# Optimization experiments

Measured on AMD Instinct MI355X. Metric: run time of the kernel, lower is better.

## Reference

```python
import jax, jax.numpy as jnp
import numpy as np

H = 512          # size_half
K = 16           # n_segments
B = 8192         # batch
WIDTH = 1.0 / K  # spline bin width


def setup_inputs() -> dict:
    key = jax.random.key(0)
    ks = jax.random.split(key, 4)
    v_in = jax.random.uniform(ks[0], (B, 2 * H), dtype=jnp.float32)  # config in [0,1]
    log_density = jax.random.normal(ks[1], (B, 1), dtype=jnp.float32)
    W1 = jax.random.normal(ks[2], (H, H), dtype=jnp.float32) * (1.0 / np.sqrt(H))
    b1 = jnp.zeros((H,), dtype=jnp.float32)
    W2 = jax.random.normal(ks[3], (H, H * K), dtype=jnp.float32) * (1.0 / np.sqrt(H))
    b2 = jnp.zeros((H * K,), dtype=jnp.float32)
    return {"v_in": v_in, "log_density": log_density, "W1": W1, "b1": b1, "W2": W2, "b2": b2}


def reference(v_in, log_density, W1, b1, W2, b2):
    # even_sites=True: passive = first half, active = second half
    v_passive = v_in[:, :H]           # [B, H]
    v_active = v_in[:, H:]            # [B, H]

    # FullyConnectedNeuralNetwork: hidden layer + final layer, tanh activation on both
    h = jnp.tanh((v_passive - 0.5) @ W1 + b1)          # [B, H]
    net = jnp.tanh(h @ W2 + b2).reshape(-1, H, K)      # [B, H, K]
    p = jax.nn.softmax(net, axis=2)                    # bin probability masses P_k

    # y-coordinates of knots: CDF of the bin masses, with leading zero
    knots_y = jnp.concatenate(
        [jnp.zeros((p.shape[0], H, 1), p.dtype), jnp.cumsum(p, axis=2)], axis=2
    )                                                  # [B, H, K+1]

    # searchsorted on uniform knots linspace(0,1,K+1), then -1, clamped
    knots_x = jnp.linspace(0.0, 1.0, K + 1, dtype=v_in.dtype)
    k = jnp.clip(jnp.searchsorted(knots_x, v_active, side="left") - 1, 0, K - 1)  # [B, H]

    p_k = jnp.take_along_axis(p, k[..., None], axis=2)[..., 0]        # [B, H]
    y_lo = jnp.take_along_axis(knots_y, k[..., None], axis=2)[..., 0]  # [B, H]

    alpha = (v_active - k.astype(v_in.dtype) * WIDTH) / WIDTH          # [B, H]
    v_out_active = y_lo + alpha * p_k

    v_out = jnp.concatenate([v_passive, v_out_active], axis=1)         # [B, 2H]
    log_density_out = log_density - jnp.sum(jnp.log(p_k), axis=1, keepdims=True)  # [B, 1]
    return v_out, log_density_out
```

## Files before the change

### kernel.cpp

```cpp
#include <hip/hip_runtime.h>
#include <hip/hip_bf16.h>

#define HH   512
#define BB   8192
#define WIDTH (1.0f/16.0f)

typedef __attribute__((ext_vector_type(8))) short  short8;
typedef __attribute__((ext_vector_type(4))) float  floatx4;

typedef const __attribute__((address_space(1))) void* gptr_t;
typedef __attribute__((address_space(3))) void*       lptr_t;

__device__ __forceinline__ void gload_lds16(const void* g, void* l) {
    __builtin_amdgcn_global_load_lds((gptr_t)g, (lptr_t)l, 16, 0, 0);
}

__device__ __forceinline__ float tanh_fast(float x) {
    float e = __expf(2.0f * x);
    return 1.0f - 2.0f * __builtin_amdgcn_rcpf(e + 1.0f);
}

__global__ void prep_all(const float* __restrict__ vin, const float* __restrict__ W1,
                         const float* __restrict__ W2, const float* __restrict__ ld,
                         float* __restrict__ vout, float* __restrict__ ldout,
                         __hip_bfloat16* __restrict__ Abf,
                         __hip_bfloat16* __restrict__ W1T,
                         __hip_bfloat16* __restrict__ W2T) {
    __shared__ float tile[32][33];
    int bid = blockIdx.x, tid = threadIdx.x;
    if (bid < 4352) {
        const float* src;  __hip_bfloat16* dst;  int cols, c0, r0;
        if (bid < 4096) { src = W2; dst = W2T; cols = 8192; c0 = (bid & 255) * 32; r0 = (bid >> 8) * 32; }
        else            { int b = bid - 4096; src = W1; dst = W1T; cols = 512; c0 = (b & 15) * 32; r0 = (b >> 4) * 32; }
        int x = tid & 31, y = tid >> 5;
        #pragma unroll
        for (int i = 0; i < 32; i += 8)
            tile[y + i][x] = src[(size_t)(r0 + y + i) * cols + c0 + x];
        __syncthreads();
        #pragma unroll
        for (int i = 0; i < 32; i += 8)
            dst[(size_t)(c0 + y + i) * 512 + r0 + x] = __float2bfloat16(tile[x][y + i]);
    } else {
        int b = bid - 4352;
        int i = b * 256 + tid;
        int r = i >> 6, c = i & 63;
        const float4* src = (const float4*)(vin + (size_t)r * 1024 + c * 8);
        float4 f0 = src[0], f1 = src[1];
        float4* dst = (float4*)(vout + (size_t)r * 1024 + c * 8);
        dst[0] = f0; dst[1] = f1;
        union { __hip_bfloat16 h[8]; uint4 v; } u;
        u.h[0] = __float2bfloat16(f0.x - 0.5f); u.h[1] = __float2bfloat16(f0.y - 0.5f);
        u.h[2] = __float2bfloat16(f0.z - 0.5f); u.h[3] = __float2bfloat16(f0.w - 0.5f);
        u.h[4] = __float2bfloat16(f1.x - 0.5f); u.h[5] = __float2bfloat16(f1.y - 0.5f);
        u.h[6] = __float2bfloat16(f1.z - 0.5f); u.h[7] = __float2bfloat16(f1.w - 0.5f);
        *(uint4*)(Abf + (size_t)r * 512 + c * 8) = u.v;
        if (tid < 4) { int row = b * 4 + tid; ldout[row] = ld[row]; }
    }
}

__global__ __launch_bounds__(256, 4) void gemm1_kernel(
        const __hip_bfloat16* __restrict__ Abf,
        const __hip_bfloat16* __restrict__ W1T,
        const float* __restrict__ b1,
        __hip_bfloat16* __restrict__ hM) {
    __shared__ short ldsA[64 * 32];
    __shared__ short ldsB[128 * 32];
    int tid = threadIdx.x;
    int lane = tid & 63;
    int wv = tid >> 6, wr = wv >> 1, wc = wv & 1;
    int q = lane >> 4, cx = lane & 15;
    int rowBase = blockIdx.y * 64;
    int colBase = blockIdx.x * 128;
    floatx4 acc[2][4] = {};

    for (int k0 = 0; k0 < HH; k0 += 32) {
        {
            int row = tid >> 2, kc = tid & 3;
            unsigned loff = __builtin_amdgcn_readfirstlane((unsigned)((tid & 192) * 16));
            gload_lds16(Abf + (size_t)(rowBase + row) * HH + k0 + kc * 8, (char*)ldsA + loff);
        }
        #pragma unroll
        for (int j = 0; j < 2; ++j) {
            int i = j * 256 + tid;
            int row = i >> 2, kc = i & 3;
            unsigned loff = __builtin_amdgcn_readfirstlane((unsigned)((j * 256 + (tid & 192)) * 16));
            gload_lds16(W1T + (size_t)(colBase + row) * HH + k0 + kc * 8, (char*)ldsB + loff);
        }
        __syncthreads();
        short8 a[2], b[4];
        #pragma unroll
        for (int mt = 0; mt < 2; ++mt)
            a[mt] = *(const short8*)(ldsA + (wr * 32 + mt * 16 + cx) * 32 + q * 8);
        #pragma unroll
        for (int nt = 0; nt < 4; ++nt)
            b[nt] = *(const short8*)(ldsB + (wc * 64 + nt * 16 + cx) * 32 + q * 8);
        #pragma unroll
        for (int mt = 0; mt < 2; ++mt)
            #pragma unroll
            for (int nt = 0; nt < 4; ++nt)
                acc[mt][nt] = __builtin_amdgcn_mfma_f32_16x16x32_bf16(a[mt], b[nt], acc[mt][nt], 0, 0, 0);
        __syncthreads();
    }

    float b1v[4];
    #pragma unroll
    for (int nt = 0; nt < 4; ++nt) b1v[nt] = b1[colBase + wc * 64 + nt * 16 + cx];
    #pragma unroll
    for (int mt = 0; mt < 2; ++mt)
        #pragma unroll
        for (int nt = 0; nt < 4; ++nt) {
            int col = colBase + wc * 64 + nt * 16 + cx;
            #pragma unroll
            for (int r = 0; r < 4; ++r) {
                int row = rowBase + wr * 32 + mt * 16 + q * 4 + r;
                hM[(size_t)row * HH + col] = __float2bfloat16(tanh_fast(acc[mt][nt][r] + b1v[nt]));
            }
        }
}

__global__ __launch_bounds__(256, 4) void gemm2_kernel(
        const __hip_bfloat16* __restrict__ hM,
        const __hip_bfloat16* __restrict__ W2T,
        const float* __restrict__ b2,
        const float* __restrict__ vin,
        float* __restrict__ vout,
        float* __restrict__ ldout) {
    __shared__ __align__(16) char smem[32768];
    short* ldsA = (short*)smem;
    short* ldsB = (short*)(smem + 16384);
    float* ldsE = (float*)smem;
    int tid = threadIdx.x;
    int lane = tid & 63;
    int wv = tid >> 6, wr = wv >> 1, wc = wv & 1;
    int q = lane >> 4, cx = lane & 15;
    int rowBase = blockIdx.y * 128;
    int colBase = blockIdx.x * 128;
    floatx4 acc[4][4] = {};

    int aoff = (q ^ (cx & 3)) * 8;

    for (int k0 = 0; k0 < HH; k0 += 64) {
        #pragma unroll
        for (int j = 0; j < 4; ++j) {
            int chunk = j * 256 + tid;
            int half  = j >> 1;
            int c2    = chunk & 511;
            int row = c2 >> 2, kc = c2 & 3;
            int kcs = kc ^ (row & 3);
            unsigned loff = __builtin_amdgcn_readfirstlane((unsigned)((j * 256 + (tid & 192)) * 16));
            gload_lds16(hM  + (size_t)(rowBase + row) * HH + k0 + half * 32 + kcs * 8, (char*)ldsA + loff);
            gload_lds16(W2T + (size_t)(colBase + row) * HH + k0 + half * 32 + kcs * 8, (char*)ldsB + loff);
        }
        __syncthreads();
        #pragma unroll
        for (int s = 0; s < 2; ++s) {
            const short* pA = ldsA + s * 4096;
            const short* pB = ldsB + s * 4096;
            short8 a[4], b[4];
            #pragma unroll
            for (int mt = 0; mt < 4; ++mt)
                a[mt] = *(const short8*)(pA + (wr * 64 + mt * 16 + cx) * 32 + aoff);
            #pragma unroll
            for (int nt = 0; nt < 4; ++nt)
                b[nt] = *(const short8*)(pB + (wc * 64 + nt * 16 + cx) * 32 + aoff);
            #pragma unroll
            for (int mt = 0; mt < 4; ++mt)
                #pragma unroll
                for (int nt = 0; nt < 4; ++nt)
                    acc[mt][nt] = __builtin_amdgcn_mfma_f32_16x16x32_bf16(a[mt], b[nt], acc[mt][nt], 0, 0, 0);
        }
        __syncthreads();
    }

    float b2v[4];
    #pragma unroll
    for (int nt = 0; nt < 4; ++nt) b2v[nt] = b2[colBase + wc * 64 + nt * 16 + cx];

    float* myTile = ldsE + wv * (16 * 68);
    int rowL  = lane & 15;
    int gL    = lane >> 4;
    int gAbs  = blockIdx.x * 8 + wc * 4 + gL;

    #pragma unroll
    for (int mt = 0; mt < 4; ++mt) {
        #pragma unroll
        for (int nt = 0; nt < 4; ++nt)
            #pragma unroll
            for (int r = 0; r < 4; ++r)
                myTile[(q * 4 + r) * 68 + nt * 16 + cx] = acc[mt][nt][r] + b2v[nt];

        floatx4 x0 = *(const floatx4*)(myTile + rowL * 68 + gL * 16);
        floatx4 x1 = *(const floatx4*)(myTile + rowL * 68 + gL * 16 + 4);
        floatx4 x2 = *(const floatx4*)(myTile + rowL * 68 + gL * 16 + 8);
        floatx4 x3 = *(const floatx4*)(myTile + rowL * 68 + gL * 16 + 12);
        float xs[16] = { x0[0],x0[1],x0[2],x0[3], x1[0],x1[1],x1[2],x1[3],
                         x2[0],x2[1],x2[2],x2[3], x3[0],x3[1],x3[2],x3[3] };

        int row = rowBase + wr * 64 + mt * 16 + rowL;
        float v = vin[(size_t)row * 1024 + 512 + gAbs];
        int k = (int)ceilf(v * 16.0f) - 1;
        k = min(15, max(0, k));

        float s = 0.0f, csum = 0.0f, ek = 0.0f;
        #pragma unroll
        for (int j = 0; j < 16; ++j) {
            float e2 = __expf(2.0f * xs[j]);
            float t  = 1.0f - 2.0f * __builtin_amdgcn_rcpf(e2 + 1.0f);
            float e  = __expf(t);
            csum += (j < k)  ? e : 0.0f;
            ek    = (j == k) ? e : ek;
            s += e;
        }
        float rs = __builtin_amdgcn_rcpf(s);
        float pk  = ek * rs;
        float ylo = csum * rs;
        float alpha = (v - (float)k * WIDTH) * 16.0f;
        vout[(size_t)row * 1024 + 512 + gAbs] = ylo + alpha * pk;

        float logp = __logf(pk);
        logp += __shfl_xor(logp, 16, 64);
        logp += __shfl_xor(logp, 32, 64);
        if (lane < 16) atomicAdd(ldout + row, -logp);
    }
}

extern "C" void kernel_launch(void* const* d_in, const int* in_sizes, int n_in,
                              void* d_out, int out_size, void* d_ws, size_t ws_size,
                              hipStream_t stream) {
    const float* vin = (const float*)d_in[0];
    const float* ld  = (const float*)d_in[1];
    const float* W1  = (const float*)d_in[2];
    const float* b1  = (const float*)d_in[3];
    const float* W2  = (const float*)d_in[4];
    const float* b2  = (const float*)d_in[5];
    float* vout  = (float*)d_out;
    float* ldout = vout + (size_t)BB * 1024;

    char* ws = (char*)d_ws;
    __hip_bfloat16* Abf = (__hip_bfloat16*)(ws);
    __hip_bfloat16* W1T = (__hip_bfloat16*)(ws + 8388608);
    __hip_bfloat16* W2T = (__hip_bfloat16*)(ws + 8912896);
    __hip_bfloat16* hM  = (__hip_bfloat16*)(ws + 17301504);

    prep_all<<<6400, 256, 0, stream>>>(vin, W1, W2, ld, vout, ldout, Abf, W1T, W2T);
    gemm1_kernel<<<dim3(4, 128), 256, 0, stream>>>(Abf, W1T, b1, hM);
    gemm2_kernel<<<dim3(64, 64), 256, 0, stream>>>(hM, W2T, b2, vin, vout, ldout);
}
```

Before: 207.4 us.

## Use 32x32 MFMA in gemm2 and replace log-density atomics with partial-sum reduction

```diff
diff --git a/kernel.cpp b/kernel.cpp
--- a/kernel.cpp
+++ b/kernel.cpp
@@ -5,8 +5,9 @@
 #define BB   8192
 #define WIDTH (1.0f/16.0f)
 
-typedef __attribute__((ext_vector_type(8))) short  short8;
-typedef __attribute__((ext_vector_type(4))) float  floatx4;
+typedef __attribute__((ext_vector_type(8)))  short short8;
+typedef __attribute__((ext_vector_type(4)))  float floatx4;
+typedef __attribute__((ext_vector_type(16))) float floatx16;
 
 typedef const __attribute__((address_space(1))) void* gptr_t;
 typedef __attribute__((address_space(3))) void*       lptr_t;
@@ -21,8 +22,8 @@
 }
 
 __global__ void prep_all(const float* __restrict__ vin, const float* __restrict__ W1,
-                         const float* __restrict__ W2, const float* __restrict__ ld,
-                         float* __restrict__ vout, float* __restrict__ ldout,
+                         const float* __restrict__ W2,
+                         float* __restrict__ vout,
                          __hip_bfloat16* __restrict__ Abf,
                          __hip_bfloat16* __restrict__ W1T,
                          __hip_bfloat16* __restrict__ W2T) {
@@ -54,7 +55,6 @@
         u.h[4] = __float2bfloat16(f1.x - 0.5f); u.h[5] = __float2bfloat16(f1.y - 0.5f);
         u.h[6] = __float2bfloat16(f1.z - 0.5f); u.h[7] = __float2bfloat16(f1.w - 0.5f);
         *(uint4*)(Abf + (size_t)r * 512 + c * 8) = u.v;
-        if (tid < 4) { int row = b * 4 + tid; ldout[row] = ld[row]; }
     }
 }
 
@@ -124,20 +124,20 @@
         const float* __restrict__ b2,
         const float* __restrict__ vin,
         float* __restrict__ vout,
-        float* __restrict__ ldout) {
-    __shared__ __align__(16) char smem[32768];
+        float* __restrict__ partial) {
+    __shared__ __align__(16) char smem[34816];
     short* ldsA = (short*)smem;
     short* ldsB = (short*)(smem + 16384);
     float* ldsE = (float*)smem;
     int tid = threadIdx.x;
     int lane = tid & 63;
     int wv = tid >> 6, wr = wv >> 1, wc = wv & 1;
-    int q = lane >> 4, cx = lane & 15;
+    int m31 = lane & 31, q2 = lane >> 5;
     int rowBase = blockIdx.y * 128;
     int colBase = blockIdx.x * 128;
-    floatx4 acc[4][4] = {};
-
-    int aoff = (q ^ (cx & 3)) * 8;
+    floatx16 acc[2][2] = {};
+
+    int key = (lane & 3);
 
     for (int k0 = 0; k0 < HH; k0 += 64) {
         #pragma unroll
@@ -145,83 +145,102 @@
             int chunk = j * 256 + tid;
             int half  = j >> 1;
             int c2    = chunk & 511;
-            int row = c2 >> 2, kc = c2 & 3;
-            int kcs = kc ^ (row & 3);
+            int row = c2 >> 2, slot = c2 & 3;
+            int kcs = slot ^ (row & 3);
             unsigned loff = __builtin_amdgcn_readfirstlane((unsigned)((j * 256 + (tid & 192)) * 16));
             gload_lds16(hM  + (size_t)(rowBase + row) * HH + k0 + half * 32 + kcs * 8, (char*)ldsA + loff);
             gload_lds16(W2T + (size_t)(colBase + row) * HH + k0 + half * 32 + kcs * 8, (char*)ldsB + loff);
         }
         __syncthreads();
         #pragma unroll
-        for (int s = 0; s < 2; ++s) {
-            const short* pA = ldsA + s * 4096;
-            const short* pB = ldsB + s * 4096;
-            short8 a[4], b[4];
-            #pragma unroll
-            for (int mt = 0; mt < 4; ++mt)
-                a[mt] = *(const short8*)(pA + (wr * 64 + mt * 16 + cx) * 32 + aoff);
-            #pragma unroll
-            for (int nt = 0; nt < 4; ++nt)
-                b[nt] = *(const short8*)(pB + (wc * 64 + nt * 16 + cx) * 32 + aoff);
-            #pragma unroll
-            for (int mt = 0; mt < 4; ++mt)
+        for (int h = 0; h < 2; ++h) {
+            const short* pA = ldsA + h * 4096;
+            const short* pB = ldsB + h * 4096;
+            #pragma unroll
+            for (int s = 0; s < 2; ++s) {
+                int slot = (s * 2 + q2) ^ key;
+                short8 a[2], b[2];
                 #pragma unroll
-                for (int nt = 0; nt < 4; ++nt)
-                    acc[mt][nt] = __builtin_amdgcn_mfma_f32_16x16x32_bf16(a[mt], b[nt], acc[mt][nt], 0, 0, 0);
-        }
-        __syncthreads();
-    }
-
-    float b2v[4];
-    #pragma unroll
-    for (int nt = 0; nt < 4; ++nt) b2v[nt] = b2[colBase + wc * 64 + nt * 16 + cx];
-
-    float* myTile = ldsE + wv * (16 * 68);
-    int rowL  = lane & 15;
-    int gL    = lane >> 4;
-    int gAbs  = blockIdx.x * 8 + wc * 4 + gL;
-
-    #pragma unroll
-    for (int mt = 0; mt < 4; ++mt) {
-        #pragma unroll
-        for (int nt = 0; nt < 4; ++nt)
-            #pragma unroll
-            for (int r = 0; r < 4; ++r)
-                myTile[(q * 4 + r) * 68 + nt * 16 + cx] = acc[mt][nt][r] + b2v[nt];
-
-        floatx4 x0 = *(const floatx4*)(myTile + rowL * 68 + gL * 16);
-        floatx4 x1 = *(const floatx4*)(myTile + rowL * 68 + gL * 16 + 4);
-        floatx4 x2 = *(const floatx4*)(myTile + rowL * 68 + gL * 16 + 8);
-        floatx4 x3 = *(const floatx4*)(myTile + rowL * 68 + gL * 16 + 12);
-        float xs[16] = { x0[0],x0[1],x0[2],x0[3], x1[0],x1[1],x1[2],x1[3],
-                         x2[0],x2[1],x2[2],x2[3], x3[0],x3[1],x3[2],x3[3] };
-
-        int row = rowBase + wr * 64 + mt * 16 + rowL;
-        float v = vin[(size_t)row * 1024 + 512 + gAbs];
-        int k = (int)ceilf(v * 16.0f) - 1;
-        k = min(15, max(0, k));
-
-        float s = 0.0f, csum = 0.0f, ek = 0.0f;
-        #pragma unroll
-        for (int j = 0; j < 16; ++j) {
-            float e2 = __expf(2.0f * xs[j]);
-            float t  = 1.0f - 2.0f * __builtin_amdgcn_rcpf(e2 + 1.0f);
-            float e  = __expf(t);
-            csum += (j < k)  ? e : 0.0f;
-            ek    = (j == k) ? e : ek;
-            s += e;
-        }
-        float rs = __builtin_amdgcn_rcpf(s);
-        float pk  = ek * rs;
-        float ylo = csum * rs;
-        float alpha = (v - (float)k * WIDTH) * 16.0f;
-        vout[(size_t)row * 1024 + 512 + gAbs] = ylo + alpha * pk;
-
-        float logp = __logf(pk);
-        logp += __shfl_xor(logp, 16, 64);
-        logp += __shfl_xor(logp, 32, 64);
-        if (lane < 16) atomicAdd(ldout + row, -logp);
-    }
+                for (int mt = 0; mt < 2; ++mt)
+                    a[mt] = *(const short8*)(pA + (wr * 64 + mt * 32 + m31) * 32 + slot * 8);
+                #pragma unroll
+                for (int nt = 0; nt < 2; ++nt)
+                    b[nt] = *(const short8*)(pB + (wc * 64 + nt * 32 + m31) * 32 + slot * 8);
+                #pragma unroll
+                for (int mt = 0; mt < 2; ++mt)
+                    #pragma unroll
+                    for (int nt = 0; nt < 2; ++nt)
+                        acc[mt][nt] = __builtin_amdgcn_mfma_f32_32x32x16_bf16(a[mt], b[nt], acc[mt][nt], 0, 0, 0);
+            }
+        }
+        __syncthreads();
+    }
+
+    float b2v[2];
+    #pragma unroll
+    for (int nt = 0; nt < 2; ++nt) b2v[nt] = b2[colBase + wc * 64 + nt * 32 + m31];
+
+    float* myTile = ldsE + wv * (32 * 68);
+
+    #pragma unroll
+    for (int mt = 0; mt < 2; ++mt) {
+        #pragma unroll
+        for (int nt = 0; nt < 2; ++nt)
+            #pragma unroll
+            for (int reg = 0; reg < 16; ++reg) {
+                int r = (reg & 3) + 8 * (reg >> 2) + 4 * q2;
+                myTile[r * 68 + nt * 32 + m31] = acc[mt][nt][reg] + b2v[nt];
+            }
+
+        float lpsum = 0.0f;
+        #pragma unroll
+        for (int gi = 0; gi < 2; ++gi) {
+            int g = q2 * 2 + gi;
+            floatx4 x0 = *(const floatx4*)(myTile + m31 * 68 + g * 16);
+            floatx4 x1 = *(const floatx4*)(myTile + m31 * 68 + g * 16 + 4);
+            floatx4 x2 = *(const floatx4*)(myTile + m31 * 68 + g * 16 + 8);
+            floatx4 x3 = *(const floatx4*)(myTile + m31 * 68 + g * 16 + 12);
+            float xs[16] = { x0[0],x0[1],x0[2],x0[3], x1[0],x1[1],x1[2],x1[3],
+                             x2[0],x2[1],x2[2],x2[3], x3[0],x3[1],x3[2],x3[3] };
+
+            int row  = rowBase + wr * 64 + mt * 32 + m31;
+            int gAbs = blockIdx.x * 8 + wc * 4 + g;
+            float v = vin[(size_t)row * 1024 + 512 + gAbs];
+            int k = (int)ceilf(v * 16.0f) - 1;
+            k = min(15, max(0, k));
+
+            float s = 0.0f, csum = 0.0f, ek = 0.0f;
+            #pragma unroll
+            for (int j = 0; j < 16; ++j) {
+                float e2 = __expf(2.0f * xs[j]);
+                float t  = 1.0f - 2.0f * __builtin_amdgcn_rcpf(e2 + 1.0f);
+                float e  = __expf(t);
+                csum += (j < k)  ? e : 0.0f;
+                ek    = (j == k) ? e : ek;
+                s += e;
+            }
+            float rs = __builtin_amdgcn_rcpf(s);
+            float pk  = ek * rs;
+            float ylo = csum * rs;
+            float alpha = (v - (float)k * WIDTH) * 16.0f;
+            vout[(size_t)row * 1024 + 512 + gAbs] = ylo + alpha * pk;
+            lpsum += __logf(pk);
+        }
+        int row = rowBase + wr * 64 + mt * 32 + m31;
+        lpsum += __shfl_xor(lpsum, 32, 64);
+        if (lane < 32) partial[(size_t)row * 128 + blockIdx.x * 2 + wc] = lpsum;
+    }
+}
+
+__global__ void finish_logdens(const float* __restrict__ partial,
+                               const float* __restrict__ ld,
+                               float* __restrict__ out) {
+    int wv = threadIdx.x >> 6, lane = threadIdx.x & 63;
+    int row = blockIdx.x * 4 + wv;
+    float s = partial[(size_t)row * 128 + lane] + partial[(size_t)row * 128 + 64 + lane];
+    #pragma unroll
+    for (int d = 32; d > 0; d >>= 1) s += __shfl_down(s, d, 64);
+    if (lane == 0) out[row] = ld[row] - s;
 }
 
 extern "C" void kernel_launch(void* const* d_in, const int* in_sizes, int n_in,
@@ -241,8 +260,10 @@
     __hip_bfloat16* W1T = (__hip_bfloat16*)(ws + 8388608);
     __hip_bfloat16* W2T = (__hip_bfloat16*)(ws + 8912896);
     __hip_bfloat16* hM  = (__hip_bfloat16*)(ws + 17301504);
-
-    prep_all<<<6400, 256, 0, stream>>>(vin, W1, W2, ld, vout, ldout, Abf, W1T, W2T);
+    float* partial = (float*)(ws + 25690112);
+
+    prep_all<<<6400, 256, 0, stream>>>(vin, W1, W2, vout, Abf, W1T, W2T);
     gemm1_kernel<<<dim3(4, 128), 256, 0, stream>>>(Abf, W1T, b1, hM);
-    gemm2_kernel<<<dim3(64, 64), 256, 0, stream>>>(hM, W2T, b2, vin, vout, ldout);
-}
+    gemm2_kernel<<<dim3(64, 64), 256, 0, stream>>>(hM, W2T, b2, vin, vout, partial);
+    finish_logdens<<<2048, 256, 0, stream>>>(partial, ld, ldout);
+}
```

Measured after the change: 212.8 us. +2.6%, slower.
